# Kernel tuning notes

Hardware: AMD Instinct MI355X
Metric: run time of the kernel (lower is better)

## Reference

```python
import jax, jax.numpy as jnp
import numpy as np
import math

VOCAB = 32000
DIM = 1024
TOKENS = 4096
PAD_IDX = 0
NBITS = 4
QN = -(2 ** (NBITS - 1))        # -8
QP = 2 ** (NBITS - 1) - 1       # 7


def setup_inputs() -> dict:
    key = jax.random.key(0)
    k_idx, k_w = jax.random.split(key)
    idx = jax.random.randint(k_idx, (TOKENS,), 0, VOCAB)
    # x is one-hot over the vocabulary, as implied by topk(x,1)[1] extracting the index
    x = jax.nn.one_hot(idx, VOCAB, dtype=jnp.float32)
    weight = jax.random.normal(k_w, (DIM, VOCAB), dtype=jnp.float32) * 0.02
    # LSQ init rule: alpha = 2 * mean|W| / sqrt(Qp)
    alpha = (2.0 * jnp.mean(jnp.abs(weight)) / math.sqrt(QP)).reshape(1)
    return {"x": x, "weight": weight, "alpha": alpha}


def reference(x, weight, alpha):
    # topk(x, 1)[1] on a one-hot input == argmax over vocab
    idx = jnp.argmax(x, axis=-1)                       # [T]
    mask = (idx == PAD_IDX)[:, None]                   # [T, 1]
    a = alpha[0]
    # LSQ fake-quantize the weight: round(clamp(w/alpha, Qn, Qp)) * alpha
    w_q = jnp.round(jnp.clip(weight / a, QN, QP)) * a  # [DIM, VOCAB]
    out = jnp.einsum('tv,dv->td', x, w_q)              # [T, DIM]
    return jnp.where(mask, 0.0, out)
```

## Files before the change

### kernel.cpp

```cpp
#include <hip/hip_runtime.h>


typedef float v4f __attribute__((ext_vector_type(4)));

constexpr int VOCAB  = 32000;
constexpr int DIM    = 1024;
constexpr int TOKENS = 4096;
constexpr int V4     = VOCAB / 4;
constexpr int WAVE   = 64;
constexpr int FULL_ITERS = V4 / 256;
constexpr int TAIL_BASE  = FULL_ITERS * 256;

__device__ __forceinline__ int check4(v4f v, int chunk) {
    if (v.x > 0.5f) return 4 * chunk + 0;
    if (v.y > 0.5f) return 4 * chunk + 1;
    if (v.z > 0.5f) return 4 * chunk + 2;
    if (v.w > 0.5f) return 4 * chunk + 3;
    return -1;
}

__global__ __launch_bounds__(WAVE) void emb_lsq_kernel(
    const float* __restrict__ x,
    const float* __restrict__ w,
    const float* __restrict__ alpha,
    float* __restrict__ out)
{
    const int t    = blockIdx.x;
    const int lane = threadIdx.x;

    const v4f* xr = reinterpret_cast<const v4f*>(x + (size_t)t * VOCAB);
    int found = -1;
    for (int k = 0; k < FULL_ITERS; ++k) {
        const int i = lane + 256 * k;
        v4f a0 = xr[i];
        v4f a1 = xr[i +  64];
        v4f a2 = xr[i + 128];
        v4f a3 = xr[i + 192];
        int f;
        if ((f = check4(a0, i      )) >= 0) found = f;
        else if ((f = check4(a1, i +  64)) >= 0) found = f;
        else if ((f = check4(a2, i + 128)) >= 0) found = f;
        else if ((f = check4(a3, i + 192)) >= 0) found = f;
        if (__ballot(found >= 0)) break;
    }
    if (!__ballot(found >= 0)) {
        v4f a = xr[TAIL_BASE + lane];
        found = check4(a, TAIL_BASE + lane);
    }
    unsigned long long m = __ballot(found >= 0);
    const int idx = m ? __shfl(found, (int)__ffsll(m) - 1) : -1;

    v4f* orow = reinterpret_cast<v4f*>(out + (size_t)t * DIM);
    if (idx <= 0) {
        v4f z = 0.f;
        #pragma unroll
        for (int j = 0; j < 4; ++j) orow[lane + 64 * j] = z;
    } else {
        const float a = alpha[0];
        const size_t col = (size_t)idx;
        float wv[16];
        #pragma unroll
        for (int j = 0; j < 4; ++j) {
            const int d0 = 4 * lane + 256 * j;
            wv[4*j+0] = w[(size_t)(d0 + 0) * VOCAB + col];
            wv[4*j+1] = w[(size_t)(d0 + 1) * VOCAB + col];
            wv[4*j+2] = w[(size_t)(d0 + 2) * VOCAB + col];
            wv[4*j+3] = w[(size_t)(d0 + 3) * VOCAB + col];
        }
        #pragma unroll
        for (int j = 0; j < 4; ++j) {
            v4f q;
            q.x = rintf(fminf(fmaxf(wv[4*j+0] / a, -8.f), 7.f)) * a;
            q.y = rintf(fminf(fmaxf(wv[4*j+1] / a, -8.f), 7.f)) * a;
            q.z = rintf(fminf(fmaxf(wv[4*j+2] / a, -8.f), 7.f)) * a;
            q.w = rintf(fminf(fmaxf(wv[4*j+3] / a, -8.f), 7.f)) * a;
            orow[lane + 64 * j] = q;
        }
    }
}

extern "C" void kernel_launch(void* const* d_in, const int* in_sizes, int n_in,
                              void* d_out, int out_size, void* d_ws, size_t ws_size,
                              hipStream_t stream) {
    const float* x     = (const float*)d_in[0];
    const float* w     = (const float*)d_in[1];
    const float* alpha = (const float*)d_in[2];
    float* out         = (float*)d_out;

    emb_lsq_kernel<<<TOKENS, WAVE, 0, stream>>>(x, w, alpha, out);
}
```

Before: 719.8 us.

## Split into scan and bucketed gather kernels grouping tokens by vocab column block

```diff
diff --git a/kernel.cpp b/kernel.cpp
--- a/kernel.cpp
+++ b/kernel.cpp
@@ -8,8 +8,10 @@
 constexpr int TOKENS = 4096;
 constexpr int V4     = VOCAB / 4;
 constexpr int WAVE   = 64;
-constexpr int FULL_ITERS = V4 / 256;
-constexpr int TAIL_BASE  = FULL_ITERS * 256;
+constexpr int FULL8      = V4 / 512;
+constexpr int TAIL_BASE  = FULL8 * 512;
+constexpr int BUCKET_COLS = 32;
+constexpr int NBUCKETS   = VOCAB / BUCKET_COLS;
 
 __device__ __forceinline__ int check4(v4f v, int chunk) {
     if (v.x > 0.5f) return 4 * chunk + 0;
@@ -19,62 +21,97 @@
     return -1;
 }
 
-__global__ __launch_bounds__(WAVE) void emb_lsq_kernel(
-    const float* __restrict__ x,
-    const float* __restrict__ w,
-    const float* __restrict__ alpha,
-    float* __restrict__ out)
+__global__ __launch_bounds__(WAVE) void scan_kernel(
+    const float* __restrict__ x, int* __restrict__ idxs)
 {
     const int t    = blockIdx.x;
     const int lane = threadIdx.x;
+    const v4f* xr = reinterpret_cast<const v4f*>(x + (size_t)t * VOCAB);
 
-    const v4f* xr = reinterpret_cast<const v4f*>(x + (size_t)t * VOCAB);
     int found = -1;
-    for (int k = 0; k < FULL_ITERS; ++k) {
-        const int i = lane + 256 * k;
+    for (int k = 0; k < FULL8; ++k) {
+        const int i = lane + 512 * k;
         v4f a0 = xr[i];
         v4f a1 = xr[i +  64];
         v4f a2 = xr[i + 128];
         v4f a3 = xr[i + 192];
+        v4f a4 = xr[i + 256];
+        v4f a5 = xr[i + 320];
+        v4f a6 = xr[i + 384];
+        v4f a7 = xr[i + 448];
         int f;
-        if ((f = check4(a0, i      )) >= 0) found = f;
+        if      ((f = check4(a0, i      )) >= 0) found = f;
         else if ((f = check4(a1, i +  64)) >= 0) found = f;
         else if ((f = check4(a2, i + 128)) >= 0) found = f;
         else if ((f = check4(a3, i + 192)) >= 0) found = f;
+        else if ((f = check4(a4, i + 256)) >= 0) found = f;
+        else if ((f = check4(a5, i + 320)) >= 0) found = f;
+        else if ((f = check4(a6, i + 384)) >= 0) found = f;
+        else if ((f = check4(a7, i + 448)) >= 0) found = f;
         if (__ballot(found >= 0)) break;
     }
     if (!__ballot(found >= 0)) {
-        v4f a = xr[TAIL_BASE + lane];
-        found = check4(a, TAIL_BASE + lane);
+        #pragma unroll
+        for (int j = 0; j < 5; ++j) {
+            const int c = TAIL_BASE + lane + 64 * j;
+            v4f a = xr[c];
+            int f = check4(a, c);
+            if (f >= 0) found = f;
+        }
     }
     unsigned long long m = __ballot(found >= 0);
-    const int idx = m ? __shfl(found, (int)__ffsll(m) - 1) : -1;
+    int idx = m ? __shfl(found, (int)__ffsll(m) - 1) : 0;
+    if (idx < 0) idx = 0;
+    if (lane == 0) idxs[t] = idx;
+}
 
-    v4f* orow = reinterpret_cast<v4f*>(out + (size_t)t * DIM);
-    if (idx <= 0) {
-        v4f z = 0.f;
-        #pragma unroll
-        for (int j = 0; j < 4; ++j) orow[lane + 64 * j] = z;
-    } else {
-        const float a = alpha[0];
-        const size_t col = (size_t)idx;
-        float wv[16];
-        #pragma unroll
-        for (int j = 0; j < 4; ++j) {
-            const int d0 = 4 * lane + 256 * j;
-            wv[4*j+0] = w[(size_t)(d0 + 0) * VOCAB + col];
-            wv[4*j+1] = w[(size_t)(d0 + 1) * VOCAB + col];
-            wv[4*j+2] = w[(size_t)(d0 + 2) * VOCAB + col];
-            wv[4*j+3] = w[(size_t)(d0 + 3) * VOCAB + col];
+__global__ __launch_bounds__(256) void gather_kernel(
+    const float* __restrict__ w,
+    const float* __restrict__ alpha,
+    const int* __restrict__ idxs,
+    float* __restrict__ out)
+{
+    const int b   = blockIdx.x;
+    const int tid = threadIdx.x;
+
+    __shared__ int s_cnt;
+    __shared__ int s_list[TOKENS];
+    if (tid == 0) s_cnt = 0;
+    __syncthreads();
+
+    for (int i = tid; i < TOKENS; i += 256) {
+        int id = idxs[i];
+        if ((id >> 5) == b) {
+            int p = atomicAdd(&s_cnt, 1);
+            s_list[p] = (i << 15) | id;
         }
-        #pragma unroll
-        for (int j = 0; j < 4; ++j) {
+    }
+    __syncthreads();
+
+    const int m = s_cnt;
+    if (m == 0) return;
+    const float a = alpha[0];
+
+    for (int k = 0; k < m; ++k) {
+        const int pk  = s_list[k];
+        const int t   = pk >> 15;
+        const int col = pk & 0x7fff;
+        v4f* orow = reinterpret_cast<v4f*>(out + (size_t)t * DIM);
+        if (col == 0) {
+            v4f z = 0.f;
+            orow[tid] = z;
+        } else {
+            const int d0 = 4 * tid;
+            float w0 = w[(size_t)(d0 + 0) * VOCAB + col];
+            float w1 = w[(size_t)(d0 + 1) * VOCAB + col];
+            float w2 = w[(size_t)(d0 + 2) * VOCAB + col];
+            float w3 = w[(size_t)(d0 + 3) * VOCAB + col];
             v4f q;
-            q.x = rintf(fminf(fmaxf(wv[4*j+0] / a, -8.f), 7.f)) * a;
-            q.y = rintf(fminf(fmaxf(wv[4*j+1] / a, -8.f), 7.f)) * a;
-            q.z = rintf(fminf(fmaxf(wv[4*j+2] / a, -8.f), 7.f)) * a;
-            q.w = rintf(fminf(fmaxf(wv[4*j+3] / a, -8.f), 7.f)) * a;
-            orow[lane + 64 * j] = q;
+            q.x = rintf(fminf(fmaxf(w0 / a, -8.f), 7.f)) * a;
+            q.y = rintf(fminf(fmaxf(w1 / a, -8.f), 7.f)) * a;
+            q.z = rintf(fminf(fmaxf(w2 / a, -8.f), 7.f)) * a;
+            q.w = rintf(fminf(fmaxf(w3 / a, -8.f), 7.f)) * a;
+            orow[tid] = q;
         }
     }
 }
@@ -86,6 +123,8 @@
     const float* w     = (const float*)d_in[1];
     const float* alpha = (const float*)d_in[2];
     float* out         = (float*)d_out;
+    int*   idxs        = (int*)d_ws;
 
-    emb_lsq_kernel<<<TOKENS, WAVE, 0, stream>>>(x, w, alpha, out);
+    scan_kernel<<<TOKENS, WAVE, 0, stream>>>(x, idxs);
+    gather_kernel<<<NBUCKETS, 256, 0, stream>>>(w, alpha, idxs, out);
 }
```

Measured after the change: 779.0 us. +8.2%, slower.

## Pre-quantize weights into transposed int8 codes, then gather contiguous rows

Applied to the files above, without the earlier changes.

```diff
diff --git a/kernel.cpp b/kernel.cpp
--- a/kernel.cpp
+++ b/kernel.cpp
@@ -2,6 +2,7 @@
 
 
 typedef float v4f __attribute__((ext_vector_type(4)));
+typedef int   v4i __attribute__((ext_vector_type(4)));
 
 constexpr int VOCAB  = 32000;
 constexpr int DIM    = 1024;
@@ -11,6 +12,40 @@
 constexpr int FULL_ITERS = V4 / 256;
 constexpr int TAIL_BASE  = FULL_ITERS * 256;
 
+__global__ __launch_bounds__(256) void quant_kernel(
+    const float* __restrict__ w,
+    const float* __restrict__ alpha,
+    signed char* __restrict__ codes)
+{
+    const int c0 = blockIdx.x * 32;
+    const int d0 = blockIdx.y * 128;
+    const int tid = threadIdx.x;
+    const float a = alpha[0];
+
+    __shared__ alignas(16) signed char s_tile[32][128];
+
+    const int r = tid >> 1;
+    const int p = tid & 1;
+    const v4f* wr = reinterpret_cast<const v4f*>(
+        w + (size_t)(d0 + r) * VOCAB + c0 + 16 * p);
+    #pragma unroll
+    for (int q = 0; q < 4; ++q) {
+        v4f v = wr[q];
+        const int cl = 16 * p + 4 * q;
+        s_tile[cl + 0][r] = (signed char)(int)rintf(fminf(fmaxf(v.x / a, -8.f), 7.f));
+        s_tile[cl + 1][r] = (signed char)(int)rintf(fminf(fmaxf(v.y / a, -8.f), 7.f));
+        s_tile[cl + 2][r] = (signed char)(int)rintf(fminf(fmaxf(v.z / a, -8.f), 7.f));
+        s_tile[cl + 3][r] = (signed char)(int)rintf(fminf(fmaxf(v.w / a, -8.f), 7.f));
+    }
+    __syncthreads();
+
+    const int c = tid >> 3;
+    const int k = tid & 7;
+    const v4i* src = reinterpret_cast<const v4i*>(&s_tile[c][16 * k]);
+    v4i* dst = reinterpret_cast<v4i*>(codes + (size_t)(c0 + c) * DIM + d0 + 16 * k);
+    *dst = *src;
+}
+
 __device__ __forceinline__ int check4(v4f v, int chunk) {
     if (v.x > 0.5f) return 4 * chunk + 0;
     if (v.y > 0.5f) return 4 * chunk + 1;
@@ -19,9 +54,9 @@
     return -1;
 }
 
-__global__ __launch_bounds__(WAVE) void emb_lsq_kernel(
+__global__ __launch_bounds__(WAVE) void scan_gather_kernel(
     const float* __restrict__ x,
-    const float* __restrict__ w,
+    const signed char* __restrict__ codes,
     const float* __restrict__ alpha,
     float* __restrict__ out)
 {
@@ -37,7 +72,7 @@
         v4f a2 = xr[i + 128];
         v4f a3 = xr[i + 192];
         int f;
-        if ((f = check4(a0, i      )) >= 0) found = f;
+        if      ((f = check4(a0, i      )) >= 0) found = f;
         else if ((f = check4(a1, i +  64)) >= 0) found = f;
         else if ((f = check4(a2, i + 128)) >= 0) found = f;
         else if ((f = check4(a3, i + 192)) >= 0) found = f;
@@ -48,7 +83,7 @@
         found = check4(a, TAIL_BASE + lane);
     }
     unsigned long long m = __ballot(found >= 0);
-    const int idx = m ? __shfl(found, (int)__ffsll(m) - 1) : -1;
+    const int idx = m ? __shfl(found, (int)__ffsll(m) - 1) : 0;
 
     v4f* orow = reinterpret_cast<v4f*>(out + (size_t)t * DIM);
     if (idx <= 0) {
@@ -57,23 +92,18 @@
         for (int j = 0; j < 4; ++j) orow[lane + 64 * j] = z;
     } else {
         const float a = alpha[0];
-        const size_t col = (size_t)idx;
-        float wv[16];
+        const unsigned* crow = reinterpret_cast<const unsigned*>(
+            codes + (size_t)idx * DIM);
+        unsigned u[4];
         #pragma unroll
-        for (int j = 0; j < 4; ++j) {
-            const int d0 = 4 * lane + 256 * j;
-            wv[4*j+0] = w[(size_t)(d0 + 0) * VOCAB + col];
-            wv[4*j+1] = w[(size_t)(d0 + 1) * VOCAB + col];
-            wv[4*j+2] = w[(size_t)(d0 + 2) * VOCAB + col];
-            wv[4*j+3] = w[(size_t)(d0 + 3) * VOCAB + col];
-        }
+        for (int j = 0; j < 4; ++j) u[j] = crow[lane + 64 * j];
         #pragma unroll
         for (int j = 0; j < 4; ++j) {
             v4f q;
-            q.x = rintf(fminf(fmaxf(wv[4*j+0] / a, -8.f), 7.f)) * a;
-            q.y = rintf(fminf(fmaxf(wv[4*j+1] / a, -8.f), 7.f)) * a;
-            q.z = rintf(fminf(fmaxf(wv[4*j+2] / a, -8.f), 7.f)) * a;
-            q.w = rintf(fminf(fmaxf(wv[4*j+3] / a, -8.f), 7.f)) * a;
+            q.x = (float)(signed char)(u[j]      ) * a;
+            q.y = (float)(signed char)(u[j] >>  8) * a;
+            q.z = (float)(signed char)(u[j] >> 16) * a;
+            q.w = (float)(signed char)(u[j] >> 24) * a;
             orow[lane + 64 * j] = q;
         }
     }
@@ -86,6 +116,9 @@
     const float* w     = (const float*)d_in[1];
     const float* alpha = (const float*)d_in[2];
     float* out         = (float*)d_out;
+    signed char* codes = (signed char*)d_ws;
 
-    emb_lsq_kernel<<<TOKENS, WAVE, 0, stream>>>(x, w, alpha, out);
+    dim3 qgrid(VOCAB / 32, DIM / 128);
+    quant_kernel<<<qgrid, 256, 0, stream>>>(w, alpha, codes);
+    scan_gather_kernel<<<TOKENS, WAVE, 0, stream>>>(x, codes, alpha, out);
 }
```

Result: no change. 722.5 us (+0.4%).

## Widen one-hot scan window, use integer nonzero test, pack four tokens per block

Applied to the files above, without the earlier changes.

```diff
diff --git a/kernel.cpp b/kernel.cpp
--- a/kernel.cpp
+++ b/kernel.cpp
@@ -1,54 +1,74 @@
 #include <hip/hip_runtime.h>
 
 
-typedef float v4f __attribute__((ext_vector_type(4)));
+typedef float        v4f __attribute__((ext_vector_type(4)));
+typedef unsigned int v4u __attribute__((ext_vector_type(4)));
+typedef unsigned int u32;
 
 constexpr int VOCAB  = 32000;
 constexpr int DIM    = 1024;
 constexpr int TOKENS = 4096;
 constexpr int V4     = VOCAB / 4;
-constexpr int WAVE   = 64;
-constexpr int FULL_ITERS = V4 / 256;
-constexpr int TAIL_BASE  = FULL_ITERS * 256;
+constexpr int WPT    = 8;
+constexpr int WIN    = 64 * WPT;
+constexpr int NWIN   = V4 / WIN;
+constexpr int TAILB  = NWIN * WIN;
+constexpr int TAILC  = (V4 - TAILB) / 64;
 
-__device__ __forceinline__ int check4(v4f v, int chunk) {
-    if (v.x > 0.5f) return 4 * chunk + 0;
-    if (v.y > 0.5f) return 4 * chunk + 1;
-    if (v.z > 0.5f) return 4 * chunk + 2;
-    if (v.w > 0.5f) return 4 * chunk + 3;
-    return -1;
+__device__ __forceinline__ int word_of(v4u c) {
+    return c.x ? 0 : (c.y ? 1 : (c.z ? 2 : 3));
 }
 
-__global__ __launch_bounds__(WAVE) void emb_lsq_kernel(
+__global__ __launch_bounds__(256, 8) void emb_lsq_kernel(
     const float* __restrict__ x,
     const float* __restrict__ w,
     const float* __restrict__ alpha,
     float* __restrict__ out)
 {
-    const int t    = blockIdx.x;
-    const int lane = threadIdx.x;
+    const int lane = threadIdx.x & 63;
+    const int t    = blockIdx.x * 4 + (threadIdx.x >> 6);
 
-    const v4f* xr = reinterpret_cast<const v4f*>(x + (size_t)t * VOCAB);
-    int found = -1;
-    for (int k = 0; k < FULL_ITERS; ++k) {
-        const int i = lane + 256 * k;
-        v4f a0 = xr[i];
-        v4f a1 = xr[i +  64];
-        v4f a2 = xr[i + 128];
-        v4f a3 = xr[i + 192];
-        int f;
-        if ((f = check4(a0, i      )) >= 0) found = f;
-        else if ((f = check4(a1, i +  64)) >= 0) found = f;
-        else if ((f = check4(a2, i + 128)) >= 0) found = f;
-        else if ((f = check4(a3, i + 192)) >= 0) found = f;
-        if (__ballot(found >= 0)) break;
+    const v4u* xr = reinterpret_cast<const v4u*>(x + (size_t)t * VOCAB);
+    int cand = -1;
+    for (int k = 0; k < NWIN; ++k) {
+        const int i = lane + WIN * k;
+        v4u c0 = xr[i];
+        v4u c1 = xr[i +  64];
+        v4u c2 = xr[i + 128];
+        v4u c3 = xr[i + 192];
+        v4u c4 = xr[i + 256];
+        v4u c5 = xr[i + 320];
+        v4u c6 = xr[i + 384];
+        v4u c7 = xr[i + 448];
+        u32 m0 = c0.x | c0.y | c0.z | c0.w;
+        u32 m1 = c1.x | c1.y | c1.z | c1.w;
+        u32 m2 = c2.x | c2.y | c2.z | c2.w;
+        u32 m3 = c3.x | c3.y | c3.z | c3.w;
+        u32 m4 = c4.x | c4.y | c4.z | c4.w;
+        u32 m5 = c5.x | c5.y | c5.z | c5.w;
+        u32 m6 = c6.x | c6.y | c6.z | c6.w;
+        u32 m7 = c7.x | c7.y | c7.z | c7.w;
+        if      (m0) cand = 4 * (i      ) + word_of(c0);
+        else if (m1) cand = 4 * (i +  64) + word_of(c1);
+        else if (m2) cand = 4 * (i + 128) + word_of(c2);
+        else if (m3) cand = 4 * (i + 192) + word_of(c3);
+        else if (m4) cand = 4 * (i + 256) + word_of(c4);
+        else if (m5) cand = 4 * (i + 320) + word_of(c5);
+        else if (m6) cand = 4 * (i + 384) + word_of(c6);
+        else if (m7) cand = 4 * (i + 448) + word_of(c7);
+        if (__ballot(cand >= 0)) break;
     }
-    if (!__ballot(found >= 0)) {
-        v4f a = xr[TAIL_BASE + lane];
-        found = check4(a, TAIL_BASE + lane);
+    if (!__ballot(cand >= 0)) {
+        #pragma unroll
+        for (int j = 0; j < TAILC; ++j) {
+            const int c = TAILB + lane + 64 * j;
+            v4u v = xr[c];
+            u32 m = v.x | v.y | v.z | v.w;
+            if (cand < 0 && m) cand = 4 * c + word_of(v);
+        }
     }
-    unsigned long long m = __ballot(found >= 0);
-    const int idx = m ? __shfl(found, (int)__ffsll(m) - 1) : -1;
+    const unsigned long long msk = __ballot(cand >= 0);
+    const int idx = msk ? __shfl(cand, (int)__ffsll(msk) - 1) : 0;
 
     v4f* orow = reinterpret_cast<v4f*>(out + (size_t)t * DIM);
     if (idx <= 0) {
@@ -87,5 +107,5 @@
     const float* alpha = (const float*)d_in[2];
     float* out         = (float*)d_out;
 
-    emb_lsq_kernel<<<TOKENS, WAVE, 0, stream>>>(x, w, alpha, out);
+    emb_lsq_kernel<<<TOKENS / 4, 256, 0, stream>>>(x, w, alpha, out);
 }
```

Measured after the change: 727.2 us. Within noise of the previous version (+1.0%).
